# Optimization experiments

Hardware: AMD Instinct MI355X
Metric: run time of the kernel (lower is better)

Reference implementation:

```python
import jax, jax.numpy as jnp
import numpy as np

N = 50000        # nodes
E = 1_600_000    # edges
D_IN = 256
H = 512          # hidden_dim (uniform)
N_CONVS = 2      # n_layers - 2
D_CAT = D_IN + H        # 768, GIN MLP input
D_MID = 2 * H           # 1024
D_SUM = H * 3           # sum(hidden_dim) = 1536
D_OUT = 256
LN_EPS = 1e-5


def _leaky(x):
    return jnp.where(x > 0, x, 0.1 * x)


def _layernorm(x, g, b):
    mu = jnp.mean(x, axis=-1, keepdims=True)
    var = jnp.var(x, axis=-1, keepdims=True)
    return (x - mu) * jax.lax.rsqrt(var + LN_EPS) * g + b


def setup_inputs() -> dict:
    key = jax.random.key(0)
    ks = jax.random.split(key, 16)

    def w(k, shape):
        fan_in = shape[-2] if len(shape) >= 2 else shape[-1]
        return jax.random.normal(k, shape, jnp.float32) / np.sqrt(fan_in)

    return {
        "x": jax.random.normal(ks[0], (N, D_IN), jnp.float32),
        "edge_index": jax.random.randint(ks[1], (2, E), 0, N, jnp.int32),
        "in_w": w(ks[2], (D_IN, H)),
        "in_b": jnp.zeros((H,), jnp.float32),
        # stacked per-conv params, leading dim = N_CONVS (identical shapes)
        "w1": w(ks[3], (N_CONVS, D_CAT, D_MID)),
        "b1": jnp.zeros((N_CONVS, D_MID), jnp.float32),
        "ln_g": jnp.ones((N_CONVS, D_MID), jnp.float32),
        "ln_b": jnp.zeros((N_CONVS, D_MID), jnp.float32),
        "w2": w(ks[4], (N_CONVS, D_MID, D_MID)),
        "b2": jnp.zeros((N_CONVS, D_MID), jnp.float32),
        "w3": w(ks[5], (N_CONVS, D_MID, H)),
        "b3": jnp.zeros((N_CONVS, H), jnp.float32),
        "out_w": w(ks[6], (D_SUM, D_OUT)),
        "out_b": jnp.zeros((D_OUT,), jnp.float32),
    }


def _gin_layer(x_cat, src, dst, w1, b1, g, bt, w2, b2, w3, b3):
    # GINConv with eps=0: mlp(x + sum_{j in N(i)} x_j); messages flow src -> dst
    agg = jax.ops.segment_sum(x_cat[src], dst, num_segments=N)
    h = x_cat + agg                       # [N, D_CAT]
    h = _leaky(_layernorm(h @ w1 + b1, g, bt))
    h = _leaky(h @ w2 + b2)
    return h @ w3 + b3                    # [N, H]


def reference(x, edge_index, in_w, in_b, w1, b1, ln_g, ln_b, w2, b2, w3, b3, out_w, out_b):
    src, dst = edge_index[0], edge_index[1]
    initial_x = x
    h = x @ in_w + in_b                   # in_proj: [N, H]
    hidden_states = [h]
    for i in range(N_CONVS):
        x_cat = jnp.concatenate([initial_x, h], axis=1)   # [N, D_CAT]
        h = _gin_layer(x_cat, src, dst, w1[i], b1[i], ln_g[i], ln_b[i],
                       w2[i], b2[i], w3[i], b3[i])
        hidden_states.append(h)
    hcat = jnp.concatenate(hidden_states, axis=1)         # [N, D_SUM]
    return hcat @ out_w + out_b                           # [N, D_OUT]
```

## Files before the change

### kernel.cpp

```cpp
#include <hip/hip_runtime.h>
#include <hip/hip_bf16.h>

#define NN 50000
#define DIN 256
#define HD 512
#define DCAT 768
#define DMID 1024
#define DSUM 1536
#define DOUT 256
#define CH 19200
#define LN_EPS 1e-5f

typedef __attribute__((ext_vector_type(8))) short short8;
typedef __attribute__((ext_vector_type(4))) float f32x4;
typedef __attribute__((ext_vector_type(2))) float f32x2;

__device__ __forceinline__ unsigned short f2b(float f) {
  unsigned int u = __float_as_uint(f);
  u += 0x7FFF + ((u >> 16) & 1);
  return (unsigned short)(u >> 16);
}
__device__ __forceinline__ float b2f(unsigned short s) {
  return __uint_as_float(((unsigned int)s) << 16);
}
__device__ __forceinline__ void splitbf(float v, unsigned short& hi, unsigned short& lo) {
  hi = f2b(v);
  lo = f2b(v - b2f(hi));
}
__device__ __forceinline__ unsigned char f2e4m3(float v) {
  return (unsigned char)(__builtin_amdgcn_cvt_pk_fp8_f32(v, v, 0, false) & 0xff);
}

__global__ void sentinel_fill(float* __restrict__ out, long n, float v) {
  for (long i = (long)blockIdx.x * blockDim.x + threadIdx.x; i < n;
       i += (long)gridDim.x * blockDim.x)
    out[i] = v;
}

__global__ void cast_split8_kernel(const float* __restrict__ in,
                                   unsigned short* __restrict__ oh,
                                   unsigned short* __restrict__ ol,
                                   unsigned char* __restrict__ o8, long n4) {
  for (long i = (long)blockIdx.x * blockDim.x + threadIdx.x; i < n4;
       i += (long)gridDim.x * blockDim.x) {
    float4 v = ((const float4*)in)[i];
    ushort4 h, l;
    splitbf(v.x, h.x, l.x); splitbf(v.y, h.y, l.y);
    splitbf(v.z, h.z, l.z); splitbf(v.w, h.w, l.w);
    ((ushort4*)oh)[i] = h;
    ((ushort4*)ol)[i] = l;
    unsigned int r = __builtin_amdgcn_cvt_pk_fp8_f32(v.x, v.y, 0, false);
    r = __builtin_amdgcn_cvt_pk_fp8_f32(v.z, v.w, r, true);
    ((unsigned int*)o8)[i] = r;
  }
}

template <bool SPLIT>
__global__ void cast_transpose_kernel(const float* __restrict__ in,
                                      unsigned short* __restrict__ oh,
                                      unsigned short* __restrict__ ol, int K, int N) {
  const float* src = in + (long)blockIdx.z * K * N;
  unsigned short* dh = oh + (long)blockIdx.z * K * N;
  unsigned short* dl = SPLIT ? ol + (long)blockIdx.z * K * N : nullptr;
  __shared__ unsigned short th[32][33];
  __shared__ unsigned short tl[SPLIT ? 32 : 1][33];
  int bk = blockIdx.x * 32, bn = blockIdx.y * 32;
  int tx = threadIdx.x & 31, ty = threadIdx.x >> 5;
#pragma unroll
  for (int i = ty; i < 32; i += 8) {
    float v = src[(long)(bk + i) * N + bn + tx];
    if (SPLIT) {
      unsigned short h, l;
      splitbf(v, h, l);
      th[i][tx] = h; tl[i][tx] = l;
    } else {
      th[i][tx] = f2b(v);
    }
  }
  __syncthreads();
#pragma unroll
  for (int i = ty; i < 32; i += 8) {
    dh[(long)(bn + i) * K + bk + tx] = th[tx][i];
    if (SPLIT) dl[(long)(bn + i) * K + bk + tx] = tl[tx][i];
  }
}

__global__ void deg_kernel(const int* __restrict__ dst, int E, int* __restrict__ rowptr) {
  int i = blockIdx.x * blockDim.x + threadIdx.x;
  if (i < E) atomicAdd(&rowptr[dst[i] + 1], 1);
}

__global__ void scan_block(int* __restrict__ data, int n, int* __restrict__ sums) {
  __shared__ int tmp[2][256];
  int i = blockIdx.x * 256 + threadIdx.x;
  int v = (i < n) ? data[i] : 0;
  int pp = 0;
  tmp[0][threadIdx.x] = v;
  __syncthreads();
#pragma unroll
  for (int off = 1; off < 256; off <<= 1) {
    int t2 = tmp[pp][threadIdx.x];
    if (threadIdx.x >= off) t2 += tmp[pp][threadIdx.x - off];
    tmp[pp ^ 1][threadIdx.x] = t2;
    pp ^= 1;
    __syncthreads();
  }
  if (i < n) data[i] = tmp[pp][threadIdx.x];
  if (threadIdx.x == 255) sums[blockIdx.x] = tmp[pp][255];
}

__global__ void scan_add(int* __restrict__ data, int n, const int* __restrict__ sums) {
  int i = blockIdx.x * 256 + threadIdx.x;
  if (blockIdx.x > 0 && i < n) data[i] += sums[blockIdx.x - 1];
}

__global__ void fill_kernel(const int* __restrict__ src, const int* __restrict__ dst, int E,
                            const int* __restrict__ rowptr, int* __restrict__ cursor,
                            int* __restrict__ cols) {
  int i = blockIdx.x * blockDim.x + threadIdx.x;
  if (i < E) {
    int r = dst[i];
    int p = rowptr[r] + atomicAdd(&cursor[r], 1);
    cols[p] = src[i];
  }
}

__global__ void agg_x_kernel(const unsigned short* __restrict__ xb,
                             const unsigned char* __restrict__ x8,
                             const int* __restrict__ rowptr,
                             const int* __restrict__ cols,
                             unsigned short* __restrict__ xpart) {
  int node = blockIdx.x * 4 + (threadIdx.x >> 6);
  int lane = threadIdx.x & 63;
  ushort4 own = *((const ushort4*)(xb + (long)node * DIN) + lane);
  float s0 = b2f(own.x), s1 = b2f(own.y), s2 = b2f(own.z), s3 = b2f(own.w);
  int e0 = rowptr[node], e1 = rowptr[node + 1];
  int p = e0;
#define XACC(w)                                                   \
  {                                                               \
    f32x2 t0 = __builtin_amdgcn_cvt_pk_f32_fp8((w), false);       \
    f32x2 t1 = __builtin_amdgcn_cvt_pk_f32_fp8((w), true);        \
    s0 += t0.x; s1 += t0.y; s2 += t1.x; s3 += t1.y;               \
  }
  for (; p + 3 < e1; p += 4) {
    int j0 = cols[p], j1 = cols[p + 1], j2 = cols[p + 2], j3 = cols[p + 3];
    unsigned int a = *((const unsigned int*)(x8 + (long)j0 * DIN) + lane);
    unsigned int b = *((const unsigned int*)(x8 + (long)j1 * DIN) + lane);
    unsigned int c = *((const unsigned int*)(x8 + (long)j2 * DIN) + lane);
    unsigned int d = *((const unsigned int*)(x8 + (long)j3 * DIN) + lane);
    XACC(a); XACC(b); XACC(c); XACC(d);
  }
  for (; p < e1; p++) {
    unsigned int a = *((const unsigned int*)(x8 + (long)cols[p] * DIN) + lane);
    XACC(a);
  }
#undef XACC
  ushort4 o;
  o.x = f2b(s0); o.y = f2b(s1); o.z = f2b(s2); o.w = f2b(s3);
  *((ushort4*)(xpart + (long)node * DIN) + lane) = o;
}

__global__ void agg_h_kernel(const unsigned short* __restrict__ h,
                             const unsigned char* __restrict__ h8,
                             const int* __restrict__ rowptr, const int* __restrict__ cols,
                             unsigned short* __restrict__ hpart) {
  int node = blockIdx.x * 4 + (threadIdx.x >> 6);
  int lane = threadIdx.x & 63;
  short8 own = *((const short8*)(h + (long)node * HD) + lane);
  float s[8];
#pragma unroll
  for (int q = 0; q < 8; q++) s[q] = b2f((unsigned short)own[q]);
  int e0 = rowptr[node], e1 = rowptr[node + 1];
  int p = e0;
#define HACC(w)                                                   \
  {                                                               \
    f32x2 t0 = __builtin_amdgcn_cvt_pk_f32_fp8((w).x, false);     \
    f32x2 t1 = __builtin_amdgcn_cvt_pk_f32_fp8((w).x, true);      \
    f32x2 t2 = __builtin_amdgcn_cvt_pk_f32_fp8((w).y, false);     \
    f32x2 t3 = __builtin_amdgcn_cvt_pk_f32_fp8((w).y, true);      \
    s[0] += t0.x; s[1] += t0.y; s[2] += t1.x; s[3] += t1.y;       \
    s[4] += t2.x; s[5] += t2.y; s[6] += t3.x; s[7] += t3.y;       \
  }
  for (; p + 3 < e1; p += 4) {
    int j0 = cols[p], j1 = cols[p + 1], j2 = cols[p + 2], j3 = cols[p + 3];
    uint2 a = *((const uint2*)(h8 + (long)j0 * HD) + lane);
    uint2 b = *((const uint2*)(h8 + (long)j1 * HD) + lane);
    uint2 c = *((const uint2*)(h8 + (long)j2 * HD) + lane);
    uint2 d = *((const uint2*)(h8 + (long)j3 * HD) + lane);
    HACC(a); HACC(b); HACC(c); HACC(d);
  }
  for (; p < e1; p++) {
    uint2 a = *((const uint2*)(h8 + (long)cols[p] * HD) + lane);
    HACC(a);
  }
#undef HACC
  short8 o;
#pragma unroll
  for (int q = 0; q < 8; q++) o[q] = (short)f2b(s[q]);
  *((short8*)(hpart + (long)node * HD) + lane) = o;
}

__global__ void ln_leaky_kernel(unsigned short* __restrict__ arr,
                                const float* __restrict__ gamma,
                                const float* __restrict__ beta) {
  int row = blockIdx.x, t = threadIdx.x;
  unsigned short* p = arr + (long)row * DMID;
  ushort4 u = ((const ushort4*)p)[t];
  float v0 = b2f(u.x), v1 = b2f(u.y), v2 = b2f(u.z), v3 = b2f(u.w);
  float s = v0 + v1 + v2 + v3;
  float sq = v0 * v0 + v1 * v1 + v2 * v2 + v3 * v3;
#pragma unroll
  for (int off = 32; off >= 1; off >>= 1) {
    s += __shfl_down(s, off, 64);
    sq += __shfl_down(sq, off, 64);
  }
  __shared__ float red[8];
  int w = t >> 6, lane = t & 63;
  if (lane == 0) { red[w] = s; red[4 + w] = sq; }
  __syncthreads();
  s = red[0] + red[1] + red[2] + red[3];
  sq = red[4] + red[5] + red[6] + red[7];
  float mean = s * (1.f / DMID);
  float var = sq * (1.f / DMID) - mean * mean;
  float rstd = rsqrtf(var + LN_EPS);
  float4 gv = ((const float4*)gamma)[t];
  float4 bv = ((const float4*)beta)[t];
  float o0 = (v0 - mean) * rstd * gv.x + bv.x;
  float o1 = (v1 - mean) * rstd * gv.y + bv.y;
  float o2 = (v2 - mean) * rstd * gv.z + bv.z;
  float o3 = (v3 - mean) * rstd * gv.w + bv.w;
  o0 = o0 > 0.f ? o0 : 0.1f * o0;
  o1 = o1 > 0.f ? o1 : 0.1f * o1;
  o2 = o2 > 0.f ? o2 : 0.1f * o2;
  o3 = o3 > 0.f ? o3 : 0.1f * o3;
  ushort4 ou;
  ou.x = f2b(o0); ou.y = f2b(o1); ou.z = f2b(o2); ou.w = f2b(o3);
  ((ushort4*)p)[t] = ou;
}

#define GLD16(src, dst)                                                          \
  __builtin_amdgcn_global_load_lds(                                              \
      (const __attribute__((address_space(1))) void*)(src),                      \
      (__attribute__((address_space(3))) void*)(dst), 16, 0, 0)

template <int WMODE, bool AL, bool BL, bool ACC, bool ACT, bool W8, int OCC, int BK>
__launch_bounds__(256, OCC)
__global__ void gemmx(const unsigned short* __restrict__ Ah,
                      const unsigned short* __restrict__ Al,
                      const unsigned short* __restrict__ A2h,
                      int lda, int lda2, int ksplit,
                      const unsigned short* __restrict__ Bh,
                      const unsigned short* __restrict__ Bl,
                      int ldb, const float* __restrict__ bias,
                      float* __restrict__ Cf,
                      unsigned short* __restrict__ Chi,
                      unsigned char* __restrict__ C8,
                      int ldc, int M, int K) {
  __shared__ __align__(16) unsigned short Ash[128 * BK];
  __shared__ __align__(16) unsigned short Asl[AL ? 128 * BK : 16];
  __shared__ __align__(16) unsigned short Bsh[128 * BK];
  __shared__ __align__(16) unsigned short Bsl[BL ? 128 * BK : 16];
  const int t = threadIdx.x;
  const int bm = blockIdx.x, bn = blockIdx.y;
  const int l = t & 63;
  const int w = t >> 6;
  const int wm = w >> 1, wn = w & 1;
  const int lrow = l & 15, lk = (l >> 4) * 8;

  f32x4 acc[4][4] = {};

  const int arow0 = bm * 128;
  const int brow0 = bn * 128;

  for (int k0 = 0; k0 < K; k0 += BK) {
    const bool first = k0 < ksplit;
    const unsigned short* Abase = first ? Ah : A2h;
    const int acol = first ? k0 : (k0 - ksplit);
    const int alda = first ? lda : lda2;
    __syncthreads();
#pragma unroll
    for (int it = 0; it < BK / 16; it++) {
      int c = t + it * 256;
      int row = c / (BK / 8);
      int sk = (c % (BK / 8)) * 8;
      int ar = arow0 + row;
      if (ar >= M) ar = M - 1;
      long boff = (long)(brow0 + row) * ldb + k0 + sk;
      int ldst = row * BK + sk;
      GLD16(Abase + (long)ar * alda + acol + sk, Ash + ldst);
      if (AL) GLD16(Al + (long)ar * lda + k0 + sk, Asl + ldst);
      GLD16(Bh + boff, Bsh + ldst);
      if (BL) GLD16(Bl + boff, Bsl + ldst);
    }
    __syncthreads();
#pragma unroll
    for (int kk = 0; kk < BK / 32; kk++) {
      short8 ah[4], al4[4], bh[4], bl4[4];
#pragma unroll
      for (int m = 0; m < 4; m++) {
        int ro = (wm * 64 + m * 16 + lrow) * BK + kk * 32 + lk;
        ah[m] = *(const short8*)(Ash + ro);
        if (AL) al4[m] = *(const short8*)(Asl + ro);
      }
#pragma unroll
      for (int n = 0; n < 4; n++) {
        int ro = (wn * 64 + n * 16 + lrow) * BK + kk * 32 + lk;
        bh[n] = *(const short8*)(Bsh + ro);
        if (BL) bl4[n] = *(const short8*)(Bsl + ro);
      }
#pragma unroll
      for (int m = 0; m < 4; m++)
#pragma unroll
        for (int n = 0; n < 4; n++) {
          acc[m][n] = __builtin_amdgcn_mfma_f32_16x16x32_bf16(ah[m], bh[n], acc[m][n], 0, 0, 0);
          if (BL)
            acc[m][n] = __builtin_amdgcn_mfma_f32_16x16x32_bf16(ah[m], bl4[n], acc[m][n], 0, 0, 0);
          if (AL)
            acc[m][n] = __builtin_amdgcn_mfma_f32_16x16x32_bf16(al4[m], bh[n], acc[m][n], 0, 0, 0);
        }
    }
  }

  const int orow0 = bm * 128 + wm * 64 + (l >> 4) * 4;
  const int ocol0 = bn * 128 + wn * 64 + lrow;
#pragma unroll
  for (int n = 0; n < 4; n++) {
    int gc = ocol0 + n * 16;
    float bv;
    if constexpr (ACC) bv = 0.f; else bv = bias[gc];
#pragma unroll
    for (int m = 0; m < 4; m++) {
#pragma unroll
      for (int ri = 0; ri < 4; ri++) {
        int gr = orow0 + m * 16 + ri;
        if (gr < M) {
          float v = acc[m][n][ri] + bv;
          if constexpr (ACC) v += Cf[(long)gr * ldc + gc];
          if constexpr (ACT) v = v > 0.f ? v : 0.1f * v;
          if constexpr (WMODE == 0) {
            Cf[(long)gr * ldc + gc] = v;
          } else {
            Chi[(long)gr * ldc + gc] = f2b(v);
            if constexpr (W8) C8[(long)gr * ldc + gc] = f2e4m3(v);
          }
        }
      }
    }
  }
}

extern "C" void kernel_launch(void* const* d_in, const int* in_sizes, int n_in,
                              void* d_out, int out_size, void* d_ws, size_t ws_size,
                              hipStream_t stream) {
  const float* x = (const float*)d_in[0];
  const int* ei = (const int*)d_in[1];
  const int E = in_sizes[1] / 2;
  const int* src = ei;
  const int* dst = ei + E;
  const float* in_w = (const float*)d_in[2];
  const float* in_b = (const float*)d_in[3];
  const float* w1 = (const float*)d_in[4];
  const float* b1 = (const float*)d_in[5];
  const float* ln_g = (const float*)d_in[6];
  const float* ln_b = (const float*)d_in[7];
  const float* w2 = (const float*)d_in[8];
  const float* b2 = (const float*)d_in[9];
  const float* w3 = (const float*)d_in[10];
  const float* b3 = (const float*)d_in[11];
  const float* out_w = (const float*)d_in[12];
  const float* out_b = (const float*)d_in[13];
  float* out = (float*)d_out;

  char* ws = (char*)d_ws;
  size_t off = 0;
  auto alloc = [&](size_t bytes) -> void* {
    void* p = ws + off;
    off += (bytes + 255) & ~(size_t)255;
    return p;
  };
  int* rowptr = (int*)alloc((NN + 1) * 4);
  int* cursor = (int*)alloc((size_t)NN * 4);
  int* cols = (int*)alloc((size_t)E * 4);
  int* sums = (int*)alloc(1024);
  int* sums2 = (int*)alloc(256);
  unsigned short* in_wb_h = (unsigned short*)alloc((size_t)HD * DIN * 2);
  unsigned short* in_wb_l = (unsigned short*)alloc((size_t)HD * DIN * 2);
  unsigned short* w1b = (unsigned short*)alloc(2ul * DMID * DCAT * 2);
  unsigned short* w2b = (unsigned short*)alloc(2ul * DMID * DMID * 2);
  unsigned short* w3b = (unsigned short*)alloc(2ul * HD * DMID * 2);
  unsigned short* out_wb_h = (unsigned short*)alloc((size_t)DOUT * DSUM * 2);
  unsigned short* out_wb_l = (unsigned short*)alloc((size_t)DOUT * DSUM * 2);
  unsigned short* xpart = (unsigned short*)alloc((size_t)NN * DIN * 2);
  unsigned short* h = (unsigned short*)alloc((size_t)NN * HD * 2);
  unsigned char* h8 = (unsigned char*)alloc((size_t)NN * HD);
  unsigned short* hpart = (unsigned short*)alloc((size_t)NN * HD * 2);
  unsigned short* h1c = (unsigned short*)alloc((size_t)CH * DMID * 2);
  unsigned short* h2c = (unsigned short*)alloc((size_t)CH * DMID * 2);
  const size_t need = off;

  if (need > ws_size) {
    sentinel_fill<<<2048, 256, 0, stream>>>(out, (long)NN * DOUT, (float)ws_size);
    return;
  }

  unsigned short* xb_h = hpart;
  unsigned short* xb_l = hpart + (size_t)NN * DIN;
  unsigned char* x8 = (unsigned char*)h1c;

  hipMemsetAsync(rowptr, 0, (NN + 1) * 4, stream);
  hipMemsetAsync(cursor, 0, (size_t)NN * 4, stream);

  const int eb = (E + 255) / 256;
  const int nscan = NN + 1;
  const int nsb = (nscan + 255) / 256;

  deg_kernel<<<eb, 256, 0, stream>>>(dst, E, rowptr);
  scan_block<<<nsb, 256, 0, stream>>>(rowptr, nscan, sums);
  scan_block<<<1, 256, 0, stream>>>(sums, nsb, sums2);
  scan_add<<<nsb, 256, 0, stream>>>(rowptr, nscan, sums);
  fill_kernel<<<eb, 256, 0, stream>>>(src, dst, E, rowptr, cursor, cols);

  cast_split8_kernel<<<2048, 256, 0, stream>>>(x, xb_h, xb_l, x8, (long)NN * DIN / 4);
  cast_transpose_kernel<true><<<dim3(DIN / 32, HD / 32, 1), 256, 0, stream>>>(in_w, in_wb_h, in_wb_l, DIN, HD);
  cast_transpose_kernel<false><<<dim3(DCAT / 32, DMID / 32, 2), 256, 0, stream>>>(w1, w1b, nullptr, DCAT, DMID);
  cast_transpose_kernel<false><<<dim3(DMID / 32, DMID / 32, 2), 256, 0, stream>>>(w2, w2b, nullptr, DMID, DMID);
  cast_transpose_kernel<false><<<dim3(DMID / 32, HD / 32, 2), 256, 0, stream>>>(w3, w3b, nullptr, DMID, HD);
  cast_transpose_kernel<true><<<dim3(DSUM / 32, DOUT / 32, 1), 256, 0, stream>>>(out_w, out_wb_h, out_wb_l, DSUM, DOUT);

  const int MT = (NN + 127) / 128;
  const int AGB = NN / 4;

  gemmx<1, true, true, false, false, true, 2, 32><<<dim3(MT, HD / 128), 256, 0, stream>>>(
      xb_h, xb_l, xb_h, DIN, DIN, 1 << 30, in_wb_h, in_wb_l, DIN, in_b,
      nullptr, h, h8, HD, NN, DIN);

  agg_x_kernel<<<AGB, 256, 0, stream>>>(xb_h, x8, rowptr, cols, xpart);

  gemmx<0, false, true, false, false, false, 2, 32><<<dim3(MT, DOUT / 128), 256, 0, stream>>>(
      h, nullptr, h, HD, HD, 1 << 30, out_wb_h, out_wb_l, DSUM, out_b,
      out, nullptr, nullptr, DOUT, NN, HD);

  for (int i = 0; i < 2; i++) {
    agg_h_kernel<<<AGB, 256, 0, stream>>>(h, h8, rowptr, cols, hpart);

    for (int r0 = 0; r0 < NN; r0 += CH) {
      int Mc = NN - r0 < CH ? NN - r0 : CH;
      int MTc = (Mc + 127) / 128;
      gemmx<1, false, false, false, false, false, 3, 64><<<dim3(MTc, DMID / 128), 256, 0, stream>>>(
          xpart + (size_t)r0 * DIN, nullptr, hpart + (size_t)r0 * HD, DIN, HD, DIN,
          w1b + (size_t)i * DMID * DCAT, nullptr, DCAT,
          b1 + i * DMID, nullptr, h1c, nullptr, DMID, Mc, DCAT);
      ln_leaky_kernel<<<Mc, 256, 0, stream>>>(h1c, ln_g + i * DMID, ln_b + i * DMID);
      gemmx<1, false, false, false, true, false, 3, 64><<<dim3(MTc, DMID / 128), 256, 0, stream>>>(
          h1c, nullptr, h1c, DMID, DMID, 1 << 30,
          w2b + (size_t)i * DMID * DMID, nullptr, DMID,
          b2 + i * DMID, nullptr, h2c, nullptr, DMID, Mc, DMID);
      gemmx<1, false, false, false, false, true, 3, 64><<<dim3(MTc, HD / 128), 256, 0, stream>>>(
          h2c, nullptr, h2c, DMID, DMID, 1 << 30,
          w3b + (size_t)i * HD * DMID, nullptr, DMID,
          b3 + i * HD, nullptr, h + (size_t)r0 * HD, h8 + (size_t)r0 * HD, HD, Mc, DMID);
    }

    gemmx<0, false, true, true, false, false, 2, 32><<<dim3(MT, DOUT / 128), 256, 0, stream>>>(
        h, nullptr, h, HD, HD, 1 << 30,
        out_wb_h + (size_t)(i + 1) * HD, out_wb_l + (size_t)(i + 1) * HD, DSUM,
        nullptr, out, nullptr, nullptr, DOUT, NN, HD);
  }
}
```

Baseline: 1.929 ms.

## Add double-buffered LDS pipeline GEMM for single-precision bf16 MLP layers

Adds a new gemm1p kernel that double-buffers the A and B tiles in LDS, issuing the async global-to-LDS loads for the next K tile while MFMAs run on the current one, with one barrier per iteration. It replaces gemmx for the three bf16-only MLP GEMMs in each GIN layer. The aim is to hide global load latency behind compute. LDS use doubles to 64 KB per block and occupancy is capped at 2 rather than 3. The old gemmx loses its split-A and activation paths, which are no longer used.

```diff
diff --git a/kernel.cpp b/kernel.cpp
--- a/kernel.cpp
+++ b/kernel.cpp
@@ -243,12 +243,100 @@
       (const __attribute__((address_space(1))) void*)(src),                      \
       (__attribute__((address_space(3))) void*)(dst), 16, 0, 0)
 
-template <int WMODE, bool AL, bool BL, bool ACC, bool ACT, bool W8, int OCC, int BK>
+template <bool ACT, bool W8, int BK>
+__launch_bounds__(256, 2)
+__global__ void gemm1p(const unsigned short* __restrict__ Ah,
+                       const unsigned short* __restrict__ A2h,
+                       int lda, int lda2, int ksplit,
+                       const unsigned short* __restrict__ Bh,
+                       int ldb, const float* __restrict__ bias,
+                       unsigned short* __restrict__ Chi,
+                       unsigned char* __restrict__ C8,
+                       int ldc, int M, int K) {
+  __shared__ __align__(16) unsigned short Ash[2][128 * BK];
+  __shared__ __align__(16) unsigned short Bsh[2][128 * BK];
+  const int t = threadIdx.x;
+  const int bm = blockIdx.x, bn = blockIdx.y;
+  const int l = t & 63;
+  const int w = t >> 6;
+  const int wm = w >> 1, wn = w & 1;
+  const int lrow = l & 15, lk = (l >> 4) * 8;
+
+  f32x4 acc[4][4] = {};
+
+  const int arow0 = bm * 128;
+  const int brow0 = bn * 128;
+
+  auto STAGE = [&](int buf, int k0) {
+    const bool first = k0 < ksplit;
+    const unsigned short* Abase = first ? Ah : A2h;
+    const int acol = first ? k0 : (k0 - ksplit);
+    const int alda = first ? lda : lda2;
+#pragma unroll
+    for (int it = 0; it < BK / 16; it++) {
+      int c = t + it * 256;
+      int row = c / (BK / 8);
+      int sk = (c % (BK / 8)) * 8;
+      int ar = arow0 + row;
+      if (ar >= M) ar = M - 1;
+      int ldst = row * BK + sk;
+      GLD16(Abase + (long)ar * alda + acol + sk, Ash[buf] + ldst);
+      GLD16(Bh + (long)(brow0 + row) * ldb + k0 + sk, Bsh[buf] + ldst);
+    }
+  };
+
+  const int nt = K / BK;
+  STAGE(0, 0);
+  __syncthreads();
+  int cur = 0;
+  for (int tk = 0; tk < nt; tk++) {
+    if (tk + 1 < nt) STAGE(cur ^ 1, (tk + 1) * BK);
+#pragma unroll
+    for (int kk = 0; kk < BK / 32; kk++) {
+      short8 ah[4], bh[4];
+#pragma unroll
+      for (int m = 0; m < 4; m++)
+        ah[m] = *(const short8*)(Ash[cur] + (wm * 64 + m * 16 + lrow) * BK + kk * 32 + lk);
+#pragma unroll
+      for (int n = 0; n < 4; n++)
+        bh[n] = *(const short8*)(Bsh[cur] + (wn * 64 + n * 16 + lrow) * BK + kk * 32 + lk);
+#pragma unroll
+      for (int m = 0; m < 4; m++)
+#pragma unroll
+        for (int n = 0; n < 4; n++)
+          acc[m][n] = __builtin_amdgcn_mfma_f32_16x16x32_bf16(ah[m], bh[n], acc[m][n], 0, 0, 0);
+    }
+    __syncthreads();
+    cur ^= 1;
+  }
+
+  const int orow0 = bm * 128 + wm * 64 + (l >> 4) * 4;
+  const int ocol0 = bn * 128 + wn * 64 + lrow;
+#pragma unroll
+  for (int n = 0; n < 4; n++) {
+    int gc = ocol0 + n * 16;
+    float bv = bias[gc];
+#pragma unroll
+    for (int m = 0; m < 4; m++) {
+#pragma unroll
+      for (int ri = 0; ri < 4; ri++) {
+        int gr = orow0 + m * 16 + ri;
+        if (gr < M) {
+          float v = acc[m][n][ri] + bv;
+          if constexpr (ACT) v = v > 0.f ? v : 0.1f * v;
+          Chi[(long)gr * ldc + gc] = f2b(v);
+          if constexpr (W8) C8[(long)gr * ldc + gc] = f2e4m3(v);
+        }
+      }
+    }
+  }
+}
+
+template <int WMODE, bool AL, bool BL, bool ACC, bool W8, int OCC, int BK>
 __launch_bounds__(256, OCC)
 __global__ void gemmx(const unsigned short* __restrict__ Ah,
                       const unsigned short* __restrict__ Al,
-                      const unsigned short* __restrict__ A2h,
-                      int lda, int lda2, int ksplit,
+                      int lda,
                       const unsigned short* __restrict__ Bh,
                       const unsigned short* __restrict__ Bl,
                       int ldb, const float* __restrict__ bias,
@@ -273,10 +361,6 @@
   const int brow0 = bn * 128;
 
   for (int k0 = 0; k0 < K; k0 += BK) {
-    const bool first = k0 < ksplit;
-    const unsigned short* Abase = first ? Ah : A2h;
-    const int acol = first ? k0 : (k0 - ksplit);
-    const int alda = first ? lda : lda2;
     __syncthreads();
 #pragma unroll
     for (int it = 0; it < BK / 16; it++) {
@@ -287,7 +371,7 @@
       if (ar >= M) ar = M - 1;
       long boff = (long)(brow0 + row) * ldb + k0 + sk;
       int ldst = row * BK + sk;
-      GLD16(Abase + (long)ar * alda + acol + sk, Ash + ldst);
+      GLD16(Ah + (long)ar * lda + k0 + sk, Ash + ldst);
       if (AL) GLD16(Al + (long)ar * lda + k0 + sk, Asl + ldst);
       GLD16(Bh + boff, Bsh + ldst);
       if (BL) GLD16(Bl + boff, Bsl + ldst);
@@ -336,7 +420,6 @@
         if (gr < M) {
           float v = acc[m][n][ri] + bv;
           if constexpr (ACC) v += Cf[(long)gr * ldc + gc];
-          if constexpr (ACT) v = v > 0.f ? v : 0.1f * v;
           if constexpr (WMODE == 0) {
             Cf[(long)gr * ldc + gc] = v;
           } else {
@@ -430,14 +513,14 @@
   const int MT = (NN + 127) / 128;
   const int AGB = NN / 4;
 
-  gemmx<1, true, true, false, false, true, 2, 32><<<dim3(MT, HD / 128), 256, 0, stream>>>(
-      xb_h, xb_l, xb_h, DIN, DIN, 1 << 30, in_wb_h, in_wb_l, DIN, in_b,
+  gemmx<1, true, true, false, true, 2, 32><<<dim3(MT, HD / 128), 256, 0, stream>>>(
+      xb_h, xb_l, DIN, in_wb_h, in_wb_l, DIN, in_b,
       nullptr, h, h8, HD, NN, DIN);
 
   agg_x_kernel<<<AGB, 256, 0, stream>>>(xb_h, x8, rowptr, cols, xpart);
 
-  gemmx<0, false, true, false, false, false, 2, 32><<<dim3(MT, DOUT / 128), 256, 0, stream>>>(
-      h, nullptr, h, HD, HD, 1 << 30, out_wb_h, out_wb_l, DSUM, out_b,
+  gemmx<0, false, true, false, false, 2, 32><<<dim3(MT, DOUT / 128), 256, 0, stream>>>(
+      h, nullptr, HD, out_wb_h, out_wb_l, DSUM, out_b,
       out, nullptr, nullptr, DOUT, NN, HD);
 
   for (int i = 0; i < 2; i++) {
@@ -446,23 +529,23 @@
     for (int r0 = 0; r0 < NN; r0 += CH) {
       int Mc = NN - r0 < CH ? NN - r0 : CH;
       int MTc = (Mc + 127) / 128;
-      gemmx<1, false, false, false, false, false, 3, 64><<<dim3(MTc, DMID / 128), 256, 0, stream>>>(
-          xpart + (size_t)r0 * DIN, nullptr, hpart + (size_t)r0 * HD, DIN, HD, DIN,
-          w1b + (size_t)i * DMID * DCAT, nullptr, DCAT,
-          b1 + i * DMID, nullptr, h1c, nullptr, DMID, Mc, DCAT);
+      gemm1p<false, false, 64><<<dim3(MTc, DMID / 128), 256, 0, stream>>>(
+          xpart + (size_t)r0 * DIN, hpart + (size_t)r0 * HD, DIN, HD, DIN,
+          w1b + (size_t)i * DMID * DCAT, DCAT,
+          b1 + i * DMID, h1c, nullptr, DMID, Mc, DCAT);
       ln_leaky_kernel<<<Mc, 256, 0, stream>>>(h1c, ln_g + i * DMID, ln_b + i * DMID);
-      gemmx<1, false, false, false, true, false, 3, 64><<<dim3(MTc, DMID / 128), 256, 0, stream>>>(
-          h1c, nullptr, h1c, DMID, DMID, 1 << 30,
-          w2b + (size_t)i * DMID * DMID, nullptr, DMID,
-          b2 + i * DMID, nullptr, h2c, nullptr, DMID, Mc, DMID);
-      gemmx<1, false, false, false, false, true, 3, 64><<<dim3(MTc, HD / 128), 256, 0, stream>>>(
-          h2c, nullptr, h2c, DMID, DMID, 1 << 30,
-          w3b + (size_t)i * HD * DMID, nullptr, DMID,
-          b3 + i * HD, nullptr, h + (size_t)r0 * HD, h8 + (size_t)r0 * HD, HD, Mc, DMID);
-    }
-
-    gemmx<0, false, true, true, false, false, 2, 32><<<dim3(MT, DOUT / 128), 256, 0, stream>>>(
-        h, nullptr, h, HD, HD, 1 << 30,
+      gemm1p<true, false, 64><<<dim3(MTc, DMID / 128), 256, 0, stream>>>(
+          h1c, h1c, DMID, DMID, 1 << 30,
+          w2b + (size_t)i * DMID * DMID, DMID,
+          b2 + i * DMID, h2c, nullptr, DMID, Mc, DMID);
+      gemm1p<false, true, 64><<<dim3(MTc, HD / 128), 256, 0, stream>>>(
+          h2c, h2c, DMID, DMID, 1 << 30,
+          w3b + (size_t)i * HD * DMID, DMID,
+          b3 + i * HD, h + (size_t)r0 * HD, h8 + (size_t)r0 * HD, HD, Mc, DMID);
+    }
+
+    gemmx<0, false, true, true, false, 2, 32><<<dim3(MT, DOUT / 128), 256, 0, stream>>>(
+        h, nullptr, HD,
         out_wb_h + (size_t)(i + 1) * HD, out_wb_l + (size_t)(i + 1) * HD, DSUM,
         nullptr, out, nullptr, nullptr, DOUT, NN, HD);
   }
```

Result: slower. 2.190 ms (+13.5%).
